# Kernel optimization log

Measured on AMD Instinct MI355X. Metric: run time of the kernel, lower is better.

## Reference

```python
import jax, jax.numpy as jnp
import numpy as np

E, D, H, K, N = 8, 512, 2048, 2, 1024  # experts, d_model, d_hidden, top_k, tokens
EPS = 1e-5


def _moe_linear(x, idx, W, b):
    # x: (M, in); idx: (M,) expert id per row; W: (E, out, in); b: (E, out)
    # Brute-force: compute per-expert dense GEMMs, select via one-hot (matches
    # BruteForceMoELinear math: y[i] = x[i] @ W[idx[i]].T + b[idx[i]]).
    m = jax.nn.one_hot(idx, W.shape[0], dtype=x.dtype)  # (M, E)
    y = jnp.einsum('me,eoi,mi->mo', m, W, x)
    return y + jnp.take(b, idx, axis=0)


def _forward(inp, gate_w, gate_b, w1, b1, w2, b2, ln_w, ln_b):
    # NaiveGate: linear -> top_k -> softmax over top-k logits
    logits = inp @ gate_w.T + gate_b              # (N, E)
    top_val, top_idx = jax.lax.top_k(logits, K)   # (N, K)
    score = jax.nn.softmax(top_val, axis=-1)      # (N, K)
    # repeat_interleave tokens, dispatch to experts
    x = jnp.repeat(inp, K, axis=0)                # (N*K, D)
    idx = top_idx.reshape(-1)                     # (N*K,)
    x = _moe_linear(x, idx, w1, b1)               # (N*K, H)
    x = jax.nn.gelu(x, approximate=False)         # torch F.gelu default = erf
    x = _moe_linear(x, idx, w2, b2)               # (N*K, D)
    x = x.reshape(N, K, D)
    x = jnp.einsum('nk,nkd->nd', score, x)        # bmm((N,1,K),(N,K,D)) combine
    # post layer norm (pre_lnorm=False)
    mu = jnp.mean(x, axis=-1, keepdims=True)
    var = jnp.var(x, axis=-1, keepdims=True)
    return (x - mu) * jax.lax.rsqrt(var + EPS) * ln_w + ln_b


def setup_inputs() -> dict:
    key = jax.random.key(0)
    ks = jax.random.split(key, 8)
    s = 0.02
    return {
        'inp': jax.random.normal(ks[0], (N, D), dtype=jnp.float32),
        'gate_w': s * jax.random.normal(ks[1], (E, D), dtype=jnp.float32),
        'gate_b': jnp.zeros((E,), dtype=jnp.float32),
        'w1': s * jax.random.normal(ks[2], (E, H, D), dtype=jnp.float32),
        'b1': jnp.zeros((E, H), dtype=jnp.float32),
        'w2': s * jax.random.normal(ks[3], (E, D, H), dtype=jnp.float32),
        'b2': jnp.zeros((E, D), dtype=jnp.float32),
        'ln_w': jnp.ones((D,), dtype=jnp.float32),
        'ln_b': jnp.zeros((D,), dtype=jnp.float32),
    }


def reference(inp, gate_w, gate_b, w1, b1, w2, b2, ln_w, ln_b):
    return _forward(inp, gate_w, gate_b, w1, b1, w2, b2, ln_w, ln_b)
```

## Files before the change

### kernel.cpp

```cpp
#include <hip/hip_runtime.h>
#include <cstdint>
#include <cstddef>

typedef _Float16 half_t;
typedef _Float16 half8 __attribute__((ext_vector_type(8)));
typedef float floatx4 __attribute__((ext_vector_type(4)));

#define E_ 8
#define D_ 512
#define H_ 2048
#define NTOK 1024
#define NP 2048
#define TM 128
#define MAX_TILES 24

__device__ __forceinline__ float gelu_f(float x) {
    return 0.5f * x * (1.0f + erff(x * 0.7071067811865476f));
}

__device__ __forceinline__ void gload_lds16(const half_t* g, half_t* l) {
    __builtin_amdgcn_global_load_lds(
        (__attribute__((address_space(1))) void*)(g),
        (__attribute__((address_space(3))) void*)(l),
        16, 0, 0);
}

__global__ __launch_bounds__(256) void gate_kernel(
        const float* __restrict__ inp, const float* __restrict__ gate_w,
        const float* __restrict__ gate_b, float* __restrict__ logits) {
    int n = blockIdx.x * 4 + (threadIdx.x >> 6);
    int lane = threadIdx.x & 63;
    const floatx4* xr = (const floatx4*)(inp + (size_t)n * D_);
    floatx4 x0 = xr[lane * 2], x1 = xr[lane * 2 + 1];
    #pragma unroll
    for (int e = 0; e < E_; e++) {
        const floatx4* gr = (const floatx4*)(gate_w + (size_t)e * D_);
        floatx4 g0 = gr[lane * 2], g1 = gr[lane * 2 + 1];
        float p = x0[0]*g0[0] + x0[1]*g0[1] + x0[2]*g0[2] + x0[3]*g0[3]
                + x1[0]*g1[0] + x1[1]*g1[1] + x1[2]*g1[2] + x1[3]*g1[3];
        #pragma unroll
        for (int m = 1; m < 64; m <<= 1) p += __shfl_xor(p, m);
        if (lane == 0) logits[(size_t)n * E_ + e] = p + gate_b[e];
    }
}

__global__ __launch_bounds__(256) void plan_kernel(
        const float* __restrict__ logits, float* __restrict__ score,
        int* __restrict__ idx, int* __restrict__ pos_of_pair,
        int* __restrict__ tile_e, int* __restrict__ tile_row0,
        int* __restrict__ tile_cnt, int* __restrict__ ntiles) {
    __shared__ int cnt_s[E_], off_s[E_ + 1], cur_s[E_];
    int tid = threadIdx.x;
    if (tid < E_) { cnt_s[tid] = 0; cur_s[tid] = 0; }
    __syncthreads();
    int my_e[4][2];
    #pragma unroll
    for (int i = 0; i < 4; i++) {
        int n = tid + i * 256;
        float l[E_];
        #pragma unroll
        for (int e = 0; e < E_; e++) l[e] = logits[(size_t)n * E_ + e];
        int e0 = 0; float v0 = l[0];
        #pragma unroll
        for (int e = 1; e < E_; e++) if (l[e] > v0) { v0 = l[e]; e0 = e; }
        int e1 = -1; float v1 = -3.4e38f;
        #pragma unroll
        for (int e = 0; e < E_; e++) if (e != e0 && l[e] > v1) { v1 = l[e]; e1 = e; }
        float s1 = expf(v1 - v0);
        float den = 1.0f + s1;
        score[2 * n]     = 1.0f / den;
        score[2 * n + 1] = s1 / den;
        idx[2 * n]     = e0;
        idx[2 * n + 1] = e1;
        atomicAdd(&cnt_s[e0], 1);
        atomicAdd(&cnt_s[e1], 1);
        my_e[i][0] = e0; my_e[i][1] = e1;
    }
    __syncthreads();
    if (tid == 0) {
        int o = 0;
        #pragma unroll
        for (int e = 0; e < E_; e++) { off_s[e] = o; o += cnt_s[e]; }
        off_s[E_] = o;
        int t = 0;
        for (int e = 0; e < E_; e++) {
            int c = cnt_s[e];
            int nt = (c + TM - 1) / TM;
            for (int i = 0; i < nt; i++) {
                tile_e[t] = e;
                tile_row0[t] = off_s[e] + i * TM;
                int rem = c - i * TM;
                tile_cnt[t] = rem < TM ? rem : TM;
                t++;
            }
        }
        ntiles[0] = t;
    }
    __syncthreads();
    #pragma unroll
    for (int i = 0; i < 4; i++) {
        #pragma unroll
        for (int k = 0; k < 2; k++) {
            int p = (tid + i * 256) * 2 + k;
            int e = my_e[i][k];
            int r = atomicAdd(&cur_s[e], 1);
            pos_of_pair[p] = off_s[e] + r;
        }
    }
}

__global__ __launch_bounds__(256) void scatter_kernel(
        const float* __restrict__ inp, const int* __restrict__ pos_of_pair,
        half_t* __restrict__ Xg) {
    int p = blockIdx.x * 4 + (threadIdx.x >> 6);
    int lane = threadIdx.x & 63;
    int pos = pos_of_pair[p];
    int n = p >> 1;
    const floatx4* src = (const floatx4*)(inp + (size_t)n * D_);
    floatx4 f0 = src[lane * 2], f1 = src[lane * 2 + 1];
    half8 h = { (half_t)f0[0], (half_t)f0[1], (half_t)f0[2], (half_t)f0[3],
                (half_t)f1[0], (half_t)f1[1], (half_t)f1[2], (half_t)f1[3] };
    *(half8*)(Xg + (size_t)pos * D_ + lane * 8) = h;
}

__global__ __launch_bounds__(256) void cvt_kernel(
        const float* __restrict__ w1, const float* __restrict__ w2,
        half_t* __restrict__ W1h, half_t* __restrict__ W2h) {
    const int n8 = E_ * H_ * D_ / 8;
    int i = blockIdx.x * 256 + threadIdx.x;
    const float* src; half_t* dst; int j;
    if (i < n8) { src = w1; dst = W1h; j = i; }
    else        { src = w2; dst = W2h; j = i - n8; }
    const floatx4* s = (const floatx4*)src + (size_t)j * 2;
    floatx4 f0 = s[0], f1 = s[1];
    half8 h = { (half_t)f0[0], (half_t)f0[1], (half_t)f0[2], (half_t)f0[3],
                (half_t)f1[0], (half_t)f1[1], (half_t)f1[2], (half_t)f1[3] };
    *(half8*)(dst + (size_t)j * 8) = h;
}

__global__ __launch_bounds__(256) void gemm1_kernel(
        const half_t* __restrict__ Xg, const half_t* __restrict__ W1h,
        const float* __restrict__ b1,
        const int* __restrict__ tile_e, const int* __restrict__ tile_row0,
        const int* __restrict__ tile_cnt, const int* __restrict__ ntiles,
        half_t* __restrict__ Y1) {
    __shared__ half_t As[TM * 32];
    __shared__ half_t Bs[128 * 32];
    int t = blockIdx.x;
    if (t >= ntiles[0]) return;
    int e = tile_e[t], row0 = tile_row0[t], cnt = tile_cnt[t];
    int colbase = blockIdx.y * 128;
    int tid = threadIdx.x;
    int wave = tid >> 6, lane = tid & 63;
    int quad = lane >> 4, l16 = lane & 15;
    int wm = (wave & 1) * 64, wn = (wave >> 1) * 64;

    int acol = (tid & 3) * 8;
    const half_t* Ag0 = Xg + (size_t)(row0 + (tid >> 2)) * D_ + acol;
    const half_t* Ag1 = Ag0 + 64 * D_;
    const half_t* Bg0 = W1h + ((size_t)e * H_ + colbase + (tid >> 2)) * D_ + acol;
    const half_t* Bg1 = Bg0 + 64 * D_;
    half_t* la0 = As + tid * 8;
    half_t* la1 = As + (tid + 256) * 8;
    half_t* lb0 = Bs + tid * 8;
    half_t* lb1 = Bs + (tid + 256) * 8;

    floatx4 acc[4][4] = {};
    for (int k0 = 0; k0 < D_; k0 += 32) {
        __syncthreads();
        gload_lds16(Ag0 + k0, la0);
        gload_lds16(Ag1 + k0, la1);
        gload_lds16(Bg0 + k0, lb0);
        gload_lds16(Bg1 + k0, lb1);
        __syncthreads();
        half8 a[4], b[4];
        #pragma unroll
        for (int mi = 0; mi < 4; mi++)
            a[mi] = *(const half8*)(As + (wm + mi * 16 + l16) * 32 + quad * 8);
        #pragma unroll
        for (int ni = 0; ni < 4; ni++)
            b[ni] = *(const half8*)(Bs + (wn + ni * 16 + l16) * 32 + quad * 8);
        #pragma unroll
        for (int mi = 0; mi < 4; mi++)
            #pragma unroll
            for (int ni = 0; ni < 4; ni++)
                acc[mi][ni] = __builtin_amdgcn_mfma_f32_16x16x32_f16(a[mi], b[ni], acc[mi][ni], 0, 0, 0);
    }
    float bias[4];
    #pragma unroll
    for (int ni = 0; ni < 4; ni++)
        bias[ni] = b1[(size_t)e * H_ + colbase + wn + ni * 16 + l16];
    #pragma unroll
    for (int mi = 0; mi < 4; mi++) {
        #pragma unroll
        for (int r = 0; r < 4; r++) {
            int rr = wm + mi * 16 + quad * 4 + r;
            if (rr >= cnt) continue;
            size_t rowoff = (size_t)(row0 + rr) * H_;
            #pragma unroll
            for (int ni = 0; ni < 4; ni++) {
                float v = acc[mi][ni][r] + bias[ni];
                Y1[rowoff + colbase + wn + ni * 16 + l16] = (half_t)gelu_f(v);
            }
        }
    }
}

__global__ __launch_bounds__(256) void gemm2_kernel(
        const half_t* __restrict__ Y1, const half_t* __restrict__ W2h,
        const int* __restrict__ tile_e, const int* __restrict__ tile_row0,
        const int* __restrict__ tile_cnt, const int* __restrict__ ntiles,
        float* __restrict__ Y2p) {
    __shared__ half_t As[TM * 32];
    __shared__ half_t Bs[128 * 32];
    int t = blockIdx.x;
    if (t >= ntiles[0]) return;
    int e = tile_e[t], row0 = tile_row0[t], cnt = tile_cnt[t];
    int colbase = blockIdx.y * 128;
    int kz = blockIdx.z;
    int kzbase = kz * 512;
    int tid = threadIdx.x;
    int wave = tid >> 6, lane = tid & 63;
    int quad = lane >> 4, l16 = lane & 15;
    int wm = (wave & 1) * 64, wn = (wave >> 1) * 64;

    int acol = (tid & 3) * 8;
    const half_t* Ag0 = Y1 + (size_t)(row0 + (tid >> 2)) * H_ + kzbase + acol;
    const half_t* Ag1 = Ag0 + 64 * H_;
    const half_t* Bg0 = W2h + ((size_t)e * D_ + colbase + (tid >> 2)) * H_ + kzbase + acol;
    const half_t* Bg1 = Bg0 + 64 * H_;
    half_t* la0 = As + tid * 8;
    half_t* la1 = As + (tid + 256) * 8;
    half_t* lb0 = Bs + tid * 8;
    half_t* lb1 = Bs + (tid + 256) * 8;

    floatx4 acc[4][4] = {};
    for (int k0 = 0; k0 < 512; k0 += 32) {
        __syncthreads();
        gload_lds16(Ag0 + k0, la0);
        gload_lds16(Ag1 + k0, la1);
        gload_lds16(Bg0 + k0, lb0);
        gload_lds16(Bg1 + k0, lb1);
        __syncthreads();
        half8 a[4], b[4];
        #pragma unroll
        for (int mi = 0; mi < 4; mi++)
            a[mi] = *(const half8*)(As + (wm + mi * 16 + l16) * 32 + quad * 8);
        #pragma unroll
        for (int ni = 0; ni < 4; ni++)
            b[ni] = *(const half8*)(Bs + (wn + ni * 16 + l16) * 32 + quad * 8);
        #pragma unroll
        for (int mi = 0; mi < 4; mi++)
            #pragma unroll
            for (int ni = 0; ni < 4; ni++)
                acc[mi][ni] = __builtin_amdgcn_mfma_f32_16x16x32_f16(a[mi], b[ni], acc[mi][ni], 0, 0, 0);
    }
    #pragma unroll
    for (int mi = 0; mi < 4; mi++) {
        #pragma unroll
        for (int r = 0; r < 4; r++) {
            int rr = wm + mi * 16 + quad * 4 + r;
            if (rr >= cnt) continue;
            size_t rowoff = ((size_t)kz * NP + row0 + rr) * D_;
            #pragma unroll
            for (int ni = 0; ni < 4; ni++)
                Y2p[rowoff + colbase + wn + ni * 16 + l16] = acc[mi][ni][r];
        }
    }
}

__global__ __launch_bounds__(256) void final_kernel(
        const float* __restrict__ Y2p, const float* __restrict__ b2,
        const int* __restrict__ idx, const float* __restrict__ score,
        const int* __restrict__ pos_of_pair,
        const float* __restrict__ ln_w, const float* __restrict__ ln_b,
        float* __restrict__ out) {
    int n = blockIdx.x * 4 + (threadIdx.x >> 6);
    int lane = threadIdx.x & 63;
    int p0 = pos_of_pair[2 * n], p1 = pos_of_pair[2 * n + 1];
    int e0 = idx[2 * n], e1 = idx[2 * n + 1];
    float s0 = score[2 * n], s1 = score[2 * n + 1];

    const floatx4* b2r0 = (const floatx4*)(b2 + (size_t)e0 * D_);
    const floatx4* b2r1 = (const floatx4*)(b2 + (size_t)e1 * D_);
    floatx4 a_lo = b2r0[lane * 2], a_hi = b2r0[lane * 2 + 1];
    floatx4 c_lo = b2r1[lane * 2], c_hi = b2r1[lane * 2 + 1];
    #pragma unroll
    for (int kz = 0; kz < 4; kz++) {
        const floatx4* r0 = (const floatx4*)(Y2p + ((size_t)kz * NP + p0) * D_);
        const floatx4* r1 = (const floatx4*)(Y2p + ((size_t)kz * NP + p1) * D_);
        a_lo += r0[lane * 2]; a_hi += r0[lane * 2 + 1];
        c_lo += r1[lane * 2]; c_hi += r1[lane * 2 + 1];
    }
    floatx4 y_lo = s0 * a_lo + s1 * c_lo;
    floatx4 y_hi = s0 * a_hi + s1 * c_hi;

    float s = 0.0f, q = 0.0f;
    #pragma unroll
    for (int j = 0; j < 4; j++) {
        s += y_lo[j] + y_hi[j];
        q += y_lo[j] * y_lo[j] + y_hi[j] * y_hi[j];
    }
    #pragma unroll
    for (int m = 1; m < 64; m <<= 1) {
        s += __shfl_xor(s, m);
        q += __shfl_xor(q, m);
    }
    float mean = s * (1.0f / 512.0f);
    float var = q * (1.0f / 512.0f) - mean * mean;
    float inv = 1.0f / sqrtf(var + 1e-5f);

    const floatx4* wv = (const floatx4*)ln_w;
    const floatx4* bv = (const floatx4*)ln_b;
    floatx4 o_lo = (y_lo - mean) * inv * wv[lane * 2]     + bv[lane * 2];
    floatx4 o_hi = (y_hi - mean) * inv * wv[lane * 2 + 1] + bv[lane * 2 + 1];
    floatx4* op = (floatx4*)(out + (size_t)n * D_);
    op[lane * 2] = o_lo;
    op[lane * 2 + 1] = o_hi;
}

extern "C" void kernel_launch(void* const* d_in, const int* in_sizes, int n_in,
                              void* d_out, int out_size, void* d_ws, size_t ws_size,
                              hipStream_t stream) {
    const float* inp    = (const float*)d_in[0];
    const float* gate_w = (const float*)d_in[1];
    const float* gate_b = (const float*)d_in[2];
    const float* w1     = (const float*)d_in[3];
    const float* b1     = (const float*)d_in[4];
    const float* w2     = (const float*)d_in[5];
    const float* b2     = (const float*)d_in[6];
    const float* ln_w   = (const float*)d_in[7];
    const float* ln_b   = (const float*)d_in[8];
    float* out = (float*)d_out;

    char* ws = (char*)d_ws;
    size_t o = 0;
    auto carve = [&](size_t bytes) -> char* {
        char* p = ws + o;
        o += (bytes + 255) & ~(size_t)255;
        return p;
    };
    half_t* W1h = (half_t*)carve(sizeof(half_t) * (size_t)E_ * H_ * D_);
    half_t* W2h = (half_t*)carve(sizeof(half_t) * (size_t)E_ * D_ * H_);
    half_t* Xg  = (half_t*)carve(sizeof(half_t) * (size_t)(NP + TM) * D_);
    half_t* Y1  = (half_t*)carve(sizeof(half_t) * (size_t)(NP + TM) * H_);
    float*  Y2p = (float*)carve(sizeof(float) * 4 * (size_t)NP * D_);
    float*  logits = (float*)carve(sizeof(float) * NTOK * E_);
    float*  score  = (float*)carve(sizeof(float) * NP);
    int* idx         = (int*)carve(sizeof(int) * NP);
    int* pos_of_pair = (int*)carve(sizeof(int) * NP);
    int* tile_e      = (int*)carve(sizeof(int) * MAX_TILES);
    int* tile_row0   = (int*)carve(sizeof(int) * MAX_TILES);
    int* tile_cnt    = (int*)carve(sizeof(int) * MAX_TILES);
    int* ntiles      = (int*)carve(sizeof(int) * 1);

    gate_kernel<<<NTOK / 4, 256, 0, stream>>>(inp, gate_w, gate_b, logits);
    plan_kernel<<<1, 256, 0, stream>>>(logits, score, idx, pos_of_pair,
                                       tile_e, tile_row0, tile_cnt, ntiles);
    scatter_kernel<<<NP / 4, 256, 0, stream>>>(inp, pos_of_pair, Xg);
    cvt_kernel<<<2 * E_ * H_ * D_ / 8 / 256, 256, 0, stream>>>(w1, w2, W1h, W2h);
    gemm1_kernel<<<dim3(MAX_TILES, H_ / 128), 256, 0, stream>>>(
        Xg, W1h, b1, tile_e, tile_row0, tile_cnt, ntiles, Y1);
    gemm2_kernel<<<dim3(MAX_TILES, D_ / 128, 4), 256, 0, stream>>>(
        Y1, W2h, tile_e, tile_row0, tile_cnt, ntiles, Y2p);
    final_kernel<<<NTOK / 4, 256, 0, stream>>>(Y2p, b2, idx, score, pos_of_pair, ln_w, ln_b, out);
}
```

Measured before the change: 169.4 us.

## Double-buffer LDS with BK=64 and shrink expert row tiles to 64 rows

Both expert GEMM kernels now stage the next 64-wide K slice into a second LDS buffer while MFMAs run on the current one. This cuts the sync pairs per iteration to one and overlaps global loads with compute. The row tile shrinks from 128 to 64 (MAX_TILES 24 to 40), so ragged per-expert tiles waste less padding and the launch gets more blocks. The cost is lower B-tile reuse per block, more LDS per block, and more redundant weight loads.

Measured after the change: 171.8 us. No clear change (+1.4%).

```diff
diff --git a/kernel.cpp b/kernel.cpp
--- a/kernel.cpp
+++ b/kernel.cpp
@@ -11,8 +11,8 @@
 #define H_ 2048
 #define NTOK 1024
 #define NP 2048
-#define TM 128
-#define MAX_TILES 24
+#define TM 64
+#define MAX_TILES 40
 
 __device__ __forceinline__ float gelu_f(float x) {
     return 0.5f * x * (1.0f + erff(x * 0.7071067811865476f));
@@ -144,8 +144,8 @@
         const int* __restrict__ tile_e, const int* __restrict__ tile_row0,
         const int* __restrict__ tile_cnt, const int* __restrict__ ntiles,
         half_t* __restrict__ Y1) {
-    __shared__ half_t As[TM * 32];
-    __shared__ half_t Bs[128 * 32];
+    __shared__ half_t As[2][TM * 64];
+    __shared__ half_t Bs[2][128 * 64];
     int t = blockIdx.x;
     if (t >= ntiles[0]) return;
     int e = tile_e[t], row0 = tile_row0[t], cnt = tile_cnt[t];
@@ -153,45 +153,60 @@
     int tid = threadIdx.x;
     int wave = tid >> 6, lane = tid & 63;
     int quad = lane >> 4, l16 = lane & 15;
-    int wm = (wave & 1) * 64, wn = (wave >> 1) * 64;
-
-    int acol = (tid & 3) * 8;
-    const half_t* Ag0 = Xg + (size_t)(row0 + (tid >> 2)) * D_ + acol;
-    const half_t* Ag1 = Ag0 + 64 * D_;
-    const half_t* Bg0 = W1h + ((size_t)e * H_ + colbase + (tid >> 2)) * D_ + acol;
-    const half_t* Bg1 = Bg0 + 64 * D_;
-    half_t* la0 = As + tid * 8;
-    half_t* la1 = As + (tid + 256) * 8;
-    half_t* lb0 = Bs + tid * 8;
-    half_t* lb1 = Bs + (tid + 256) * 8;
-
-    floatx4 acc[4][4] = {};
-    for (int k0 = 0; k0 < D_; k0 += 32) {
+    int wm = (wave & 1) * 32, wn = (wave >> 1) * 64;
+
+    int srow = tid >> 3, skc = (tid & 7) * 8;
+    const half_t* Ag0 = Xg + (size_t)(row0 + srow) * D_ + skc;
+    const half_t* Ag1 = Ag0 + 32 * D_;
+    const half_t* Bg0 = W1h + ((size_t)e * H_ + colbase + srow) * D_ + skc;
+    const half_t* Bg1 = Bg0 + 32 * D_;
+    const half_t* Bg2 = Bg0 + 64 * D_;
+    const half_t* Bg3 = Bg0 + 96 * D_;
+
+    #define STAGE1(buf, k0)                                        \
+        do {                                                       \
+            gload_lds16(Ag0 + (k0), &As[buf][(size_t)tid * 8]);            \
+            gload_lds16(Ag1 + (k0), &As[buf][(size_t)(tid + 256) * 8]);    \
+            gload_lds16(Bg0 + (k0), &Bs[buf][(size_t)tid * 8]);            \
+            gload_lds16(Bg1 + (k0), &Bs[buf][(size_t)(tid + 256) * 8]);    \
+            gload_lds16(Bg2 + (k0), &Bs[buf][(size_t)(tid + 512) * 8]);    \
+            gload_lds16(Bg3 + (k0), &Bs[buf][(size_t)(tid + 768) * 8]);    \
+        } while (0)
+
+    floatx4 acc[2][4] = {};
+    STAGE1(0, 0);
+    __syncthreads();
+    int cur = 0;
+    for (int k0 = 0; k0 < D_; k0 += 64) {
+        if (k0 + 64 < D_) STAGE1(cur ^ 1, k0 + 64);
+        const half_t* Ab = &As[cur][0];
+        const half_t* Bb = &Bs[cur][0];
+        #pragma unroll
+        for (int ks = 0; ks < 2; ks++) {
+            half8 a[2], b[4];
+            #pragma unroll
+            for (int mi = 0; mi < 2; mi++)
+                a[mi] = *(const half8*)(Ab + (wm + mi * 16 + l16) * 64 + ks * 32 + quad * 8);
+            #pragma unroll
+            for (int ni = 0; ni < 4; ni++)
+                b[ni] = *(const half8*)(Bb + (wn + ni * 16 + l16) * 64 + ks * 32 + quad * 8);
+            #pragma unroll
+            for (int mi = 0; mi < 2; mi++)
+                #pragma unroll
+                for (int ni = 0; ni < 4; ni++)
+                    acc[mi][ni] = __builtin_amdgcn_mfma_f32_16x16x32_f16(a[mi], b[ni], acc[mi][ni], 0, 0, 0);
+        }
         __syncthreads();
-        gload_lds16(Ag0 + k0, la0);
-        gload_lds16(Ag1 + k0, la1);
-        gload_lds16(Bg0 + k0, lb0);
-        gload_lds16(Bg1 + k0, lb1);
-        __syncthreads();
-        half8 a[4], b[4];
-        #pragma unroll
-        for (int mi = 0; mi < 4; mi++)
-            a[mi] = *(const half8*)(As + (wm + mi * 16 + l16) * 32 + quad * 8);
-        #pragma unroll
-        for (int ni = 0; ni < 4; ni++)
-            b[ni] = *(const half8*)(Bs + (wn + ni * 16 + l16) * 32 + quad * 8);
-        #pragma unroll
-        for (int mi = 0; mi < 4; mi++)
-            #pragma unroll
-            for (int ni = 0; ni < 4; ni++)
-                acc[mi][ni] = __builtin_amdgcn_mfma_f32_16x16x32_f16(a[mi], b[ni], acc[mi][ni], 0, 0, 0);
-    }
+        cur ^= 1;
+    }
+    #undef STAGE1
+
     float bias[4];
     #pragma unroll
     for (int ni = 0; ni < 4; ni++)
         bias[ni] = b1[(size_t)e * H_ + colbase + wn + ni * 16 + l16];
     #pragma unroll
-    for (int mi = 0; mi < 4; mi++) {
+    for (int mi = 0; mi < 2; mi++) {
         #pragma unroll
         for (int r = 0; r < 4; r++) {
             int rr = wm + mi * 16 + quad * 4 + r;
@@ -211,8 +226,8 @@
         const int* __restrict__ tile_e, const int* __restrict__ tile_row0,
         const int* __restrict__ tile_cnt, const int* __restrict__ ntiles,
         float* __restrict__ Y2p) {
-    __shared__ half_t As[TM * 32];
-    __shared__ half_t Bs[128 * 32];
+    __shared__ half_t As[2][TM * 64];
+    __shared__ half_t Bs[2][128 * 64];
     int t = blockIdx.x;
     if (t >= ntiles[0]) return;
     int e = tile_e[t], row0 = tile_row0[t], cnt = tile_cnt[t];
@@ -222,41 +237,56 @@
     int tid = threadIdx.x;
     int wave = tid >> 6, lane = tid & 63;
     int quad = lane >> 4, l16 = lane & 15;
-    int wm = (wave & 1) * 64, wn = (wave >> 1) * 64;
-
-    int acol = (tid & 3) * 8;
-    const half_t* Ag0 = Y1 + (size_t)(row0 + (tid >> 2)) * H_ + kzbase + acol;
-    const half_t* Ag1 = Ag0 + 64 * H_;
-    const half_t* Bg0 = W2h + ((size_t)e * D_ + colbase + (tid >> 2)) * H_ + kzbase + acol;
-    const half_t* Bg1 = Bg0 + 64 * H_;
-    half_t* la0 = As + tid * 8;
-    half_t* la1 = As + (tid + 256) * 8;
-    half_t* lb0 = Bs + tid * 8;
-    half_t* lb1 = Bs + (tid + 256) * 8;
-
-    floatx4 acc[4][4] = {};
-    for (int k0 = 0; k0 < 512; k0 += 32) {
+    int wm = (wave & 1) * 32, wn = (wave >> 1) * 64;
+
+    int srow = tid >> 3, skc = (tid & 7) * 8;
+    const half_t* Ag0 = Y1 + (size_t)(row0 + srow) * H_ + kzbase + skc;
+    const half_t* Ag1 = Ag0 + 32 * H_;
+    const half_t* Bg0 = W2h + ((size_t)e * D_ + colbase + srow) * H_ + kzbase + skc;
+    const half_t* Bg1 = Bg0 + 32 * H_;
+    const half_t* Bg2 = Bg0 + 64 * H_;
+    const half_t* Bg3 = Bg0 + 96 * H_;
+
+    #define STAGE2(buf, k0)                                        \
+        do {                                                       \
+            gload_lds16(Ag0 + (k0), &As[buf][(size_t)tid * 8]);            \
+            gload_lds16(Ag1 + (k0), &As[buf][(size_t)(tid + 256) * 8]);    \
+            gload_lds16(Bg0 + (k0), &Bs[buf][(size_t)tid * 8]);            \
+            gload_lds16(Bg1 + (k0), &Bs[buf][(size_t)(tid + 256) * 8]);    \
+            gload_lds16(Bg2 + (k0), &Bs[buf][(size_t)(tid + 512) * 8]);    \
+            gload_lds16(Bg3 + (k0), &Bs[buf][(size_t)(tid + 768) * 8]);    \
+        } while (0)
+
+    floatx4 acc[2][4] = {};
+    STAGE2(0, 0);
+    __syncthreads();
+    int cur = 0;
+    for (int k0 = 0; k0 < 512; k0 += 64) {
+        if (k0 + 64 < 512) STAGE2(cur ^ 1, k0 + 64);
+        const half_t* Ab = &As[cur][0];
+        const half_t* Bb = &Bs[cur][0];
+        #pragma unroll
+        for (int ks = 0; ks < 2; ks++) {
+            half8 a[2], b[4];
+            #pragma unroll
+            for (int mi = 0; mi < 2; mi++)
+                a[mi] = *(const half8*)(Ab + (wm + mi * 16 + l16) * 64 + ks * 32 + quad * 8);
+            #pragma unroll
+            for (int ni = 0; ni < 4; ni++)
+                b[ni] = *(const half8*)(Bb + (wn + ni * 16 + l16) * 64 + ks * 32 + quad * 8);
+            #pragma unroll
+            for (int mi = 0; mi < 2; mi++)
+                #pragma unroll
+                for (int ni = 0; ni < 4; ni++)
+                    acc[mi][ni] = __builtin_amdgcn_mfma_f32_16x16x32_f16(a[mi], b[ni], acc[mi][ni], 0, 0, 0);
+        }
         __syncthreads();
-        gload_lds16(Ag0 + k0, la0);
-        gload_lds16(Ag1 + k0, la1);
-        gload_lds16(Bg0 + k0, lb0);
-        gload_lds16(Bg1 + k0, lb1);
-        __syncthreads();
-        half8 a[4], b[4];
-        #pragma unroll
-        for (int mi = 0; mi < 4; mi++)
-            a[mi] = *(const half8*)(As + (wm + mi * 16 + l16) * 32 + quad * 8);
-        #pragma unroll
-        for (int ni = 0; ni < 4; ni++)
-            b[ni] = *(const half8*)(Bs + (wn + ni * 16 + l16) * 32 + quad * 8);
-        #pragma unroll
-        for (int mi = 0; mi < 4; mi++)
-            #pragma unroll
-            for (int ni = 0; ni < 4; ni++)
-                acc[mi][ni] = __builtin_amdgcn_mfma_f32_16x16x32_f16(a[mi], b[ni], acc[mi][ni], 0, 0, 0);
-    }
-    #pragma unroll
-    for (int mi = 0; mi < 4; mi++) {
+        cur ^= 1;
+    }
+    #undef STAGE2
+
+    #pragma unroll
+    for (int mi = 0; mi < 2; mi++) {
         #pragma unroll
         for (int r = 0; r < 4; r++) {
             int rr = wm + mi * 16 + quad * 4 + r;
@@ -342,8 +372,8 @@
     };
     half_t* W1h = (half_t*)carve(sizeof(half_t) * (size_t)E_ * H_ * D_);
     half_t* W2h = (half_t*)carve(sizeof(half_t) * (size_t)E_ * D_ * H_);
-    half_t* Xg  = (half_t*)carve(sizeof(half_t) * (size_t)(NP + TM) * D_);
-    half_t* Y1  = (half_t*)carve(sizeof(half_t) * (size_t)(NP + TM) * H_);
+    half_t* Xg  = (half_t*)carve(sizeof(half_t) * (size_t)(NP + 128) * D_);
+    half_t* Y1  = (half_t*)carve(sizeof(half_t) * (size_t)(NP + 128) * H_);
     float*  Y2p = (float*)carve(sizeof(float) * 4 * (size_t)NP * D_);
     float*  logits = (float*)carve(sizeof(float) * NTOK * E_);
     float*  score  = (float*)carve(sizeof(float) * NP);
```
